# Kernel optimization log

Hardware: AMD Instinct MI355X
Metric: run time of the kernel (lower is better)

Reference implementation:

```python
import jax, jax.numpy as jnp
import numpy as np
from jax import lax

# The external iir2d op (fyremael/iir2d, filter_id=4) is a channel-wise recursive 2D IIR
# filter. We model it faithfully as the canonical separable zero-phase first-order IIR
# (causal then anticausal recurrence along W, then along H), with 'mirror' boundary
# handled by steady-state init (y[-1] = x[0]) and 'const' boundary by border_const.
A_DECAY = 0.5  # first-order feedback coefficient for filter_id=4


def _causal(x_t, c0, a):
    # x_t: (L, ...), scan a first-order recurrence y[t] = (1-a)*x[t] + a*y[t-1]
    b = 1.0 - a

    def step(carry, xt):
        y = b * xt + a * carry
        return y, y

    _, y = lax.scan(step, c0, x_t)
    return y


def _iir1d_last(x, a, border, border_const):
    # zero-phase: causal pass then anticausal pass along the last axis
    x_t = jnp.moveaxis(x, -1, 0)  # (L, ...)
    if border == 'mirror':
        c0 = x_t[0]
    else:
        c0 = jnp.full_like(x_t[0], border_const)
    yf = _causal(x_t, c0, a)
    yr = yf[::-1]
    if border == 'mirror':
        c1 = yr[0]
    else:
        c1 = jnp.full_like(yr[0], border_const)
    yb = _causal(yr, c1, a)[::-1]
    return jnp.moveaxis(yb, 0, -1)


def iir2d(x2d, a, border, border_const):
    # x2d: (M, H, W). Filter along W, then along H.
    y = _iir1d_last(x2d, a, border, border_const)  # rows (W axis)
    y = jnp.swapaxes(y, 1, 2)                       # (M, W, H)
    y = _iir1d_last(y, a, border, border_const)     # columns (H axis)
    return jnp.swapaxes(y, 1, 2)


def setup_inputs() -> dict:
    key = jax.random.key(0)
    kx = jax.random.fold_in(key, 1)
    x = jax.random.normal(kx, (4, 512, 512, 64), dtype=jnp.float32)
    alpha = jnp.zeros((64,), dtype=jnp.float32)  # learnable blend, init 0 => mix = 0.5
    return {"x": x, "alpha": alpha}


def reference(x, alpha):
    # y = x + sigmoid(alpha) * (IIR(x) - x), channel-wise IIR on NHWC
    n, h, w, c = x.shape
    x2d = jnp.transpose(x, (0, 3, 1, 2)).reshape((n * c, h, w))
    y2d = iir2d(x2d, A_DECAY, 'mirror', 0.0)
    y = jnp.transpose(y2d.reshape((n, c, h, w)), (0, 2, 3, 1))
    mix = jax.nn.sigmoid(alpha).reshape((1, 1, 1, -1))
    return x + mix * (y - x)
```

## Files before the change

### kernel.cpp

```cpp
#include <hip/hip_runtime.h>


typedef float f4 __attribute__((ext_vector_type(4)));

constexpr int Tc   = 32;
constexpr int Kc   = 8;
constexpr int WIN  = Tc + 2 * Kc;
constexpr int L    = 512;
constexpr int C    = 64;
constexpr int W    = 512;
constexpr int H    = 512;
constexpr int CHUNKS = L / Tc;

template<bool VERT, bool COMBINE>
__global__ __launch_bounds__(256, 2)
void iir_scan(const float* __restrict__ in, float* __restrict__ out,
              const float* __restrict__ xres, const float* __restrict__ alpha)
{
    const int lane = threadIdx.x & 63;
    const int sub  = lane >> 4;
    const int c0   = (lane & 15) << 2;
    const int gw   = blockIdx.x * 4 + (threadIdx.x >> 6);
    const int lg   = gw >> 4;
    const int w0   = (gw & (CHUNKS - 1)) * Tc;

    const int n  = lg >> 7;
    const int r4 = ((lg & 127) << 2) + sub;

    int base, stride;
    if (VERT) {
        base   = (n * H * W + r4) * C + c0;
        stride = W * C;
    } else {
        base   = (n * H + r4) * (W * C) + c0;
        stride = C;
    }
    const float* __restrict__ p = in + base;

    f4 v[WIN];
#pragma unroll
    for (int j = 0; j < WIN; ++j) {
        int w = w0 - Kc + j;
        w = min(max(w, 0), L - 1);
        v[j] = *(const f4*)(p + w * stride);
    }

    f4 carry = v[0];
#pragma unroll
    for (int j = 0; j < WIN; ++j) {
        const int w = w0 - Kc + j;
        if (w >= 0 && w < L)
            carry = 0.5f * v[j] + 0.5f * carry;
        v[j] = carry;
    }

    f4 c2 = v[WIN - 1];
#pragma unroll
    for (int j = WIN - 1; j >= Kc; --j) {
        c2 = 0.5f * v[j] + 0.5f * c2;
        v[j] = c2;
    }

    if (COMBINE) {
        const f4 av = *(const f4*)(alpha + c0);
        f4 mix;
#pragma unroll
        for (int q = 0; q < 4; ++q)
            mix[q] = 1.0f / (1.0f + __expf(-av[q]));
#pragma unroll
        for (int j = Kc; j < Kc + Tc; ++j) {
            const int idx = base + (w0 + (j - Kc)) * stride;
            const f4 xv = *(const f4*)(xres + idx);
            *(f4*)(out + idx) = xv + mix * (v[j] - xv);
        }
    } else {
#pragma unroll
        for (int j = Kc; j < Kc + Tc; ++j) {
            const int idx = base + (w0 + (j - Kc)) * stride;
            *(f4*)(out + idx) = v[j];
        }
    }
}

__global__ __launch_bounds__(256)
void iir_vpass_inplace(float* __restrict__ y, const float* __restrict__ xres,
                       const float* __restrict__ alpha)
{
    const int lane = threadIdx.x & 63;
    const int sub  = lane >> 4;
    const int c0   = (lane & 15) << 2;
    const int lg   = blockIdx.x * 4 + (threadIdx.x >> 6);
    const int n = lg >> 7;
    const int w = ((lg & 127) << 2) + sub;
    const int base   = (n * H * W + w) * C + c0;
    const int stride = W * C;

    f4 carry = *(const f4*)(y + base);
    for (int h = 0; h < H; ++h) {
        const int idx = base + h * stride;
        f4 cur = *(const f4*)(y + idx);
        carry = 0.5f * cur + 0.5f * carry;
        *(f4*)(y + idx) = carry;
    }
    const f4 av = *(const f4*)(alpha + c0);
    f4 mix;
#pragma unroll
    for (int q = 0; q < 4; ++q)
        mix[q] = 1.0f / (1.0f + __expf(-av[q]));
    f4 c2 = *(const f4*)(y + base + (H - 1) * stride);
    for (int h = H - 1; h >= 0; --h) {
        const int idx = base + h * stride;
        f4 cur = *(const f4*)(y + idx);
        c2 = 0.5f * cur + 0.5f * c2;
        const f4 xv = *(const f4*)(xres + idx);
        *(f4*)(y + idx) = xv + mix * (c2 - xv);
    }
}

extern "C" void kernel_launch(void* const* d_in, const int* in_sizes, int n_in,
                              void* d_out, int out_size, void* d_ws, size_t ws_size,
                              hipStream_t stream) {
    const float* x     = (const float*)d_in[0];
    const float* alpha = (const float*)d_in[1];
    float* out = (float*)d_out;
    float* t   = (float*)d_ws;

    const size_t imgElems = (size_t)H * W * C;
    const size_t imgBytes = imgElems * sizeof(float);
    const int    N        = 4;

    int g = (int)(ws_size / imgBytes);
    if (g > N) g = N;

    if (g >= 1) {
        for (int i0 = 0; i0 < N; i0 += g) {
            const int ni = (i0 + g <= N) ? g : (N - i0);
            const size_t off = (size_t)i0 * imgElems;
            const dim3 grid((unsigned)(ni * 512)), block(256);
            iir_scan<false, false><<<grid, block, 0, stream>>>(x + off, t, nullptr, nullptr);
            iir_scan<true,  true ><<<grid, block, 0, stream>>>(t, out + off, x + off, alpha);
        }
    } else {
        const dim3 block(256);
        iir_scan<false, false><<<dim3(4 * 512), block, 0, stream>>>(x, out, nullptr, nullptr);
        iir_vpass_inplace<<<dim3(128), block, 0, stream>>>(out, x, alpha);
    }
}
```

Before: 594.1 us.

## Switch to float2 per lane, double grid, and remap blocks XCD-aware

Each lane now handles two channels with float2 instead of four with float4, which halves the register array per thread and doubles the number of blocks. The forced two-blocks-per-CU launch bound is dropped, and block IDs are remapped so that consecutive logical blocks spread across the eight XCDs. The aim is more occupancy and latency hiding for these memory-bound scans. The cost is narrower memory accesses (8-byte instead of 16-byte) and more redundant halo loads per output.

```diff
diff --git a/kernel.cpp b/kernel.cpp
--- a/kernel.cpp
+++ b/kernel.cpp
@@ -1,7 +1,7 @@
 #include <hip/hip_runtime.h>
 
 
-typedef float f4 __attribute__((ext_vector_type(4)));
+typedef float f2 __attribute__((ext_vector_type(2)));
 
 constexpr int Tc   = 32;
 constexpr int Kc   = 8;
@@ -13,39 +13,43 @@
 constexpr int CHUNKS = L / Tc;
 
 template<bool VERT, bool COMBINE>
-__global__ __launch_bounds__(256, 2)
+__global__ __launch_bounds__(256)
 void iir_scan(const float* __restrict__ in, float* __restrict__ out,
               const float* __restrict__ xres, const float* __restrict__ alpha)
 {
+    const int nb8 = (int)gridDim.x >> 3;
+    const int bid = (int)blockIdx.x;
+    const int lb  = (bid & 7) * nb8 + (bid >> 3);
+
     const int lane = threadIdx.x & 63;
-    const int sub  = lane >> 4;
-    const int c0   = (lane & 15) << 2;
-    const int gw   = blockIdx.x * 4 + (threadIdx.x >> 6);
+    const int sub  = lane >> 5;
+    const int c0   = (lane & 31) << 1;
+    const int gw   = lb * 4 + (threadIdx.x >> 6);
     const int lg   = gw >> 4;
     const int w0   = (gw & (CHUNKS - 1)) * Tc;
 
-    const int n  = lg >> 7;
-    const int r4 = ((lg & 127) << 2) + sub;
+    const int n = lg >> 8;
+    const int r = ((lg & 255) << 1) + sub;
 
     int base, stride;
     if (VERT) {
-        base   = (n * H * W + r4) * C + c0;
+        base   = (n * H * W + r) * C + c0;
         stride = W * C;
     } else {
-        base   = (n * H + r4) * (W * C) + c0;
+        base   = (n * H + r) * (W * C) + c0;
         stride = C;
     }
     const float* __restrict__ p = in + base;
 
-    f4 v[WIN];
+    f2 v[WIN];
 #pragma unroll
     for (int j = 0; j < WIN; ++j) {
         int w = w0 - Kc + j;
         w = min(max(w, 0), L - 1);
-        v[j] = *(const f4*)(p + w * stride);
+        v[j] = *(const f2*)(p + w * stride);
     }
 
-    f4 carry = v[0];
+    f2 carry = v[0];
 #pragma unroll
     for (int j = 0; j < WIN; ++j) {
         const int w = w0 - Kc + j;
@@ -54,7 +58,7 @@
         v[j] = carry;
     }
 
-    f4 c2 = v[WIN - 1];
+    f2 c2 = v[WIN - 1];
 #pragma unroll
     for (int j = WIN - 1; j >= Kc; --j) {
         c2 = 0.5f * v[j] + 0.5f * c2;
@@ -62,22 +66,22 @@
     }
 
     if (COMBINE) {
-        const f4 av = *(const f4*)(alpha + c0);
-        f4 mix;
+        const f2 av = *(const f2*)(alpha + c0);
+        f2 mix;
 #pragma unroll
-        for (int q = 0; q < 4; ++q)
+        for (int q = 0; q < 2; ++q)
             mix[q] = 1.0f / (1.0f + __expf(-av[q]));
 #pragma unroll
         for (int j = Kc; j < Kc + Tc; ++j) {
             const int idx = base + (w0 + (j - Kc)) * stride;
-            const f4 xv = *(const f4*)(xres + idx);
-            *(f4*)(out + idx) = xv + mix * (v[j] - xv);
+            const f2 xv = *(const f2*)(xres + idx);
+            *(f2*)(out + idx) = xv + mix * (v[j] - xv);
         }
     } else {
 #pragma unroll
         for (int j = Kc; j < Kc + Tc; ++j) {
             const int idx = base + (w0 + (j - Kc)) * stride;
-            *(f4*)(out + idx) = v[j];
+            *(f2*)(out + idx) = v[j];
         }
     }
 }
@@ -87,33 +91,33 @@
                        const float* __restrict__ alpha)
 {
     const int lane = threadIdx.x & 63;
-    const int sub  = lane >> 4;
-    const int c0   = (lane & 15) << 2;
+    const int sub  = lane >> 5;
+    const int c0   = (lane & 31) << 1;
     const int lg   = blockIdx.x * 4 + (threadIdx.x >> 6);
-    const int n = lg >> 7;
-    const int w = ((lg & 127) << 2) + sub;
+    const int n = lg >> 8;
+    const int w = ((lg & 255) << 1) + sub;
     const int base   = (n * H * W + w) * C + c0;
     const int stride = W * C;
 
-    f4 carry = *(const f4*)(y + base);
+    f2 carry = *(const f2*)(y + base);
     for (int h = 0; h < H; ++h) {
         const int idx = base + h * stride;
-        f4 cur = *(const f4*)(y + idx);
+        f2 cur = *(const f2*)(y + idx);
         carry = 0.5f * cur + 0.5f * carry;
-        *(f4*)(y + idx) = carry;
+        *(f2*)(y + idx) = carry;
     }
-    const f4 av = *(const f4*)(alpha + c0);
-    f4 mix;
+    const f2 av = *(const f2*)(alpha + c0);
+    f2 mix;
 #pragma unroll
-    for (int q = 0; q < 4; ++q)
+    for (int q = 0; q < 2; ++q)
         mix[q] = 1.0f / (1.0f + __expf(-av[q]));
-    f4 c2 = *(const f4*)(y + base + (H - 1) * stride);
+    f2 c2 = *(const f2*)(y + base + (H - 1) * stride);
     for (int h = H - 1; h >= 0; --h) {
         const int idx = base + h * stride;
-        f4 cur = *(const f4*)(y + idx);
+        f2 cur = *(const f2*)(y + idx);
         c2 = 0.5f * cur + 0.5f * c2;
-        const f4 xv = *(const f4*)(xres + idx);
-        *(f4*)(y + idx) = xv + mix * (c2 - xv);
+        const f2 xv = *(const f2*)(xres + idx);
+        *(f2*)(y + idx) = xv + mix * (c2 - xv);
     }
 }
 
@@ -136,13 +140,13 @@
         for (int i0 = 0; i0 < N; i0 += g) {
             const int ni = (i0 + g <= N) ? g : (N - i0);
             const size_t off = (size_t)i0 * imgElems;
-            const dim3 grid((unsigned)(ni * 512)), block(256);
+            const dim3 grid((unsigned)(ni * 1024)), block(256);
             iir_scan<false, false><<<grid, block, 0, stream>>>(x + off, t, nullptr, nullptr);
             iir_scan<true,  true ><<<grid, block, 0, stream>>>(t, out + off, x + off, alpha);
         }
     } else {
         const dim3 block(256);
-        iir_scan<false, false><<<dim3(4 * 512), block, 0, stream>>>(x, out, nullptr, nullptr);
-        iir_vpass_inplace<<<dim3(128), block, 0, stream>>>(out, x, alpha);
+        iir_scan<false, false><<<dim3(4 * 1024), block, 0, stream>>>(x, out, nullptr, nullptr);
+        iir_vpass_inplace<<<dim3(256), block, 0, stream>>>(out, x, alpha);
     }
 }
```

Measured after the change: 605.9 us. About the same (+2.0%).
